# Kernel optimization log

Measured on AMD Instinct MI355X. Metric: run time of the kernel, lower is better.

## Reference

```python
import jax, jax.numpy as jnp
import numpy as np

B, S, D = 4, 4096, 1024
H, HEAD_DIM = 16, 192  # head_dim split into q/k/v of 64 each


def setup_inputs() -> dict:
    key = jax.random.key(0)
    k1, k2 = jax.random.split(key)
    x = jax.random.normal(k1, (B, S, D), dtype=jnp.float32)
    qkv_kernel = jax.random.normal(k2, (D, H, HEAD_DIM), dtype=jnp.float32) * (1.0 / np.sqrt(D))
    qkv_bias = jnp.zeros((H, HEAD_DIM), dtype=jnp.float32)
    return {"x": x, "qkv_kernel": qkv_kernel, "qkv_bias": qkv_bias}


def reference(x, qkv_kernel, qkv_bias):
    # DenseGeneral: [B,S,D] x [D,H,HEAD_DIM] -> [B,S,H,HEAD_DIM]
    qkv = jnp.einsum('bsd,dhf->bshf', x, qkv_kernel) + qkv_bias
    q, k, v = jnp.split(qkv, 3, axis=-1)  # each [B,S,H,64]
    # Faithful to source layout: einsum '...hqd,...hkd' batches over (B,S) and
    # attends across the HEAD axis. With H <= block_size the blockwise loop in
    # the source collapses to this single full softmax over heads.
    scale = 1.0 / jnp.sqrt(jnp.asarray(HEAD_DIM, dtype=q.dtype))  # sqrt(self.head_dim)
    scores = jnp.einsum('bshd,bsgd->bshg', q, k) * scale  # [B,S,H,H]
    weights = jax.nn.softmax(scores, axis=-1)
    out = jnp.einsum('bshg,bsgd->bshd', weights, v)  # [B,S,H,64]
    return out
```

## Files before the change

kernel.cpp:

```cpp
#include <hip/hip_runtime.h>
#include <cstdint>
#include <cstddef>

typedef unsigned short u16;
typedef __attribute__((ext_vector_type(8))) short bf16x8;
typedef __attribute__((ext_vector_type(4))) float f32x4;

__device__ inline float bl(uint32_t u){ union{float f;uint32_t i;}c; c.i = u<<16; return c.f; }
__device__ inline float bh(uint32_t u){ union{float f;uint32_t i;}c; c.i = u & 0xFFFF0000u; return c.f; }
__device__ inline u16 f2bu(float f){
  union{float f;uint32_t u;} c; c.f=f;
  uint32_t u=c.u;
  return (u16)((u + 0x7FFFu + ((u>>16)&1u))>>16);
}

#define GLOAD_LDS16(g, l) __builtin_amdgcn_global_load_lds( \
    (__attribute__((address_space(1))) void*)(g), \
    (__attribute__((address_space(3))) void*)(l), 16, 0, 0)
#define BAR() do{ asm volatile("" ::: "memory"); __builtin_amdgcn_s_barrier(); asm volatile("" ::: "memory"); }while(0)
#define WAIT_LGKM0() do{ asm volatile("s_waitcnt lgkmcnt(0)" ::: "memory"); __builtin_amdgcn_sched_barrier(0); }while(0)

__global__ __launch_bounds__(256) void k_conv_x(const float* __restrict__ X,
                                                u16* __restrict__ Xb, int n4){
  int i = blockIdx.x*256 + threadIdx.x;
  int stride = gridDim.x*256;
  for (; i < n4; i += stride){
    float4 v = ((const float4*)X)[i];
    ushort4 o;
    o.x=f2bu(v.x); o.y=f2bu(v.y); o.z=f2bu(v.z); o.w=f2bu(v.w);
    ((ushort4*)Xb)[i] = o;
  }
}

__global__ __launch_bounds__(256) void k_conv_wt(const float* __restrict__ W,
                                                 u16* __restrict__ Wt){
  __shared__ float t[32][33];
  int n0 = blockIdx.x*32, k0 = blockIdx.y*32;
  int tx = threadIdx.x & 31, ty = threadIdx.x >> 5;
  #pragma unroll
  for (int i=0;i<32;i+=8)
    t[ty+i][tx] = W[(size_t)(k0+ty+i)*3072 + n0+tx];
  __syncthreads();
  #pragma unroll
  for (int i=0;i<32;i+=8)
    Wt[(size_t)(n0+ty+i)*1024 + k0+tx] = f2bu(t[tx][ty+i]);
}

__global__ __launch_bounds__(512, 2) void k_gemm2(const u16* __restrict__ Xb,
                                                  const u16* __restrict__ Wt,
                                                  const float* __restrict__ bias,
                                                  u16* __restrict__ Q){
  __shared__ __align__(16) u16 L[65536];
  const int K = 1024, N = 3072, NT = 32;
  int b = blockIdx.x;
  int swz = (b & 7)*96 + (b >> 3);
  int bm = swz / 12, bn = swz % 12;
  int m0 = bm*256, n0 = bn*256;
  int tid = threadIdx.x, w = tid>>6, lane = tid&63, lr = lane&15, lk = lane>>4;
  int wm = w>>2, wn = w&3;

  f32x4 acc[8][4];
  #pragma unroll
  for (int i=0;i<8;i++)
    #pragma unroll
    for (int j=0;j<4;j++)
      acc[i][j] = (f32x4){0.f,0.f,0.f,0.f};

  int grow = tid>>2;
  int gcol = ((((tid&3)*16) ^ (((tid>>3)&1)<<4) ^ (((tid>>4)&1)<<5)) >> 1);
  const u16* gA0 = Xb + (size_t)(m0 + grow)*K + gcol;
  const u16* gA1 = Xb + (size_t)(m0 + 128 + grow)*K + gcol;
  const u16* gB0 = Wt + (size_t)(n0 + grow)*K + gcol;
  const u16* gB1 = Wt + (size_t)(n0 + 128 + grow)*K + gcol;

#define STG_A(j) do{ int bf=(j)&3, kof=(j)*32; \
    GLOAD_LDS16(gA0+kof, &L[((bf*4+0)<<12) + tid*8]); \
    GLOAD_LDS16(gA1+kof, &L[((bf*4+1)<<12) + tid*8]); }while(0)
#define STG_B(j) do{ int bf=(j)&3, kof=(j)*32; \
    GLOAD_LDS16(gB0+kof, &L[((bf*4+2)<<12) + tid*8]); \
    GLOAD_LDS16(gB1+kof, &L[((bf*4+3)<<12) + tid*8]); }while(0)

  const char* Lb = (const char*)L;
  int colx = (lk*16) ^ (((lr>>1)&3)*16);
  int arow = lr*64 + colx;
  int brow = ((wn&1)*64 + lr)*64 + colx;

  STG_A(0); STG_B(0);
  STG_A(1); STG_B(1);
  STG_A(2); STG_B(2);
  asm volatile("s_waitcnt vmcnt(8)" ::: "memory");
  __builtin_amdgcn_sched_barrier(0);
  BAR();

  for (int t = 0; t < NT; ++t){
    int buf = t & 3;
    int Abase = (buf*4 + wm) << 13;
    int Bbase = (buf*4 + 2 + (wn>>1)) << 13;
    bool st = (t <= NT-4);

    bf16x8 af0, af1, af2, af3, bf0, bf1, bf2, bf3;
    af0 = *(const bf16x8*)(Lb + Abase + 0*1024 + arow);
    af1 = *(const bf16x8*)(Lb + Abase + 1*1024 + arow);
    af2 = *(const bf16x8*)(Lb + Abase + 2*1024 + arow);
    af3 = *(const bf16x8*)(Lb + Abase + 3*1024 + arow);
    bf0 = *(const bf16x8*)(Lb + Bbase + 0*1024 + brow);
    bf1 = *(const bf16x8*)(Lb + Bbase + 1*1024 + brow);
    bf2 = *(const bf16x8*)(Lb + Bbase + 2*1024 + brow);
    bf3 = *(const bf16x8*)(Lb + Bbase + 3*1024 + brow);
    if (st) STG_A(t+3);
    BAR();
    WAIT_LGKM0();
    __builtin_amdgcn_s_setprio(1);
    acc[0][0] = __builtin_amdgcn_mfma_f32_16x16x32_bf16(af0, bf0, acc[0][0], 0,0,0);
    acc[0][1] = __builtin_amdgcn_mfma_f32_16x16x32_bf16(af0, bf1, acc[0][1], 0,0,0);
    acc[0][2] = __builtin_amdgcn_mfma_f32_16x16x32_bf16(af0, bf2, acc[0][2], 0,0,0);
    acc[0][3] = __builtin_amdgcn_mfma_f32_16x16x32_bf16(af0, bf3, acc[0][3], 0,0,0);
    acc[1][0] = __builtin_amdgcn_mfma_f32_16x16x32_bf16(af1, bf0, acc[1][0], 0,0,0);
    acc[1][1] = __builtin_amdgcn_mfma_f32_16x16x32_bf16(af1, bf1, acc[1][1], 0,0,0);
    acc[1][2] = __builtin_amdgcn_mfma_f32_16x16x32_bf16(af1, bf2, acc[1][2], 0,0,0);
    acc[1][3] = __builtin_amdgcn_mfma_f32_16x16x32_bf16(af1, bf3, acc[1][3], 0,0,0);
    acc[2][0] = __builtin_amdgcn_mfma_f32_16x16x32_bf16(af2, bf0, acc[2][0], 0,0,0);
    acc[2][1] = __builtin_amdgcn_mfma_f32_16x16x32_bf16(af2, bf1, acc[2][1], 0,0,0);
    acc[2][2] = __builtin_amdgcn_mfma_f32_16x16x32_bf16(af2, bf2, acc[2][2], 0,0,0);
    acc[2][3] = __builtin_amdgcn_mfma_f32_16x16x32_bf16(af2, bf3, acc[2][3], 0,0,0);
    acc[3][0] = __builtin_amdgcn_mfma_f32_16x16x32_bf16(af3, bf0, acc[3][0], 0,0,0);
    acc[3][1] = __builtin_amdgcn_mfma_f32_16x16x32_bf16(af3, bf1, acc[3][1], 0,0,0);
    acc[3][2] = __builtin_amdgcn_mfma_f32_16x16x32_bf16(af3, bf2, acc[3][2], 0,0,0);
    acc[3][3] = __builtin_amdgcn_mfma_f32_16x16x32_bf16(af3, bf3, acc[3][3], 0,0,0);
    __builtin_amdgcn_s_setprio(0);
    BAR();

    af0 = *(const bf16x8*)(Lb + Abase + 4*1024 + arow);
    af1 = *(const bf16x8*)(Lb + Abase + 5*1024 + arow);
    af2 = *(const bf16x8*)(Lb + Abase + 6*1024 + arow);
    af3 = *(const bf16x8*)(Lb + Abase + 7*1024 + arow);
    if (st) STG_B(t+3);
    BAR();
    WAIT_LGKM0();
    __builtin_amdgcn_s_setprio(1);
    acc[4][0] = __builtin_amdgcn_mfma_f32_16x16x32_bf16(af0, bf0, acc[4][0], 0,0,0);
    acc[4][1] = __builtin_amdgcn_mfma_f32_16x16x32_bf16(af0, bf1, acc[4][1], 0,0,0);
    acc[4][2] = __builtin_amdgcn_mfma_f32_16x16x32_bf16(af0, bf2, acc[4][2], 0,0,0);
    acc[4][3] = __builtin_amdgcn_mfma_f32_16x16x32_bf16(af0, bf3, acc[4][3], 0,0,0);
    acc[5][0] = __builtin_amdgcn_mfma_f32_16x16x32_bf16(af1, bf0, acc[5][0], 0,0,0);
    acc[5][1] = __builtin_amdgcn_mfma_f32_16x16x32_bf16(af1, bf1, acc[5][1], 0,0,0);
    acc[5][2] = __builtin_amdgcn_mfma_f32_16x16x32_bf16(af1, bf2, acc[5][2], 0,0,0);
    acc[5][3] = __builtin_amdgcn_mfma_f32_16x16x32_bf16(af1, bf3, acc[5][3], 0,0,0);
    acc[6][0] = __builtin_amdgcn_mfma_f32_16x16x32_bf16(af2, bf0, acc[6][0], 0,0,0);
    acc[6][1] = __builtin_amdgcn_mfma_f32_16x16x32_bf16(af2, bf1, acc[6][1], 0,0,0);
    acc[6][2] = __builtin_amdgcn_mfma_f32_16x16x32_bf16(af2, bf2, acc[6][2], 0,0,0);
    acc[6][3] = __builtin_amdgcn_mfma_f32_16x16x32_bf16(af2, bf3, acc[6][3], 0,0,0);
    acc[7][0] = __builtin_amdgcn_mfma_f32_16x16x32_bf16(af3, bf0, acc[7][0], 0,0,0);
    acc[7][1] = __builtin_amdgcn_mfma_f32_16x16x32_bf16(af3, bf1, acc[7][1], 0,0,0);
    acc[7][2] = __builtin_amdgcn_mfma_f32_16x16x32_bf16(af3, bf2, acc[7][2], 0,0,0);
    acc[7][3] = __builtin_amdgcn_mfma_f32_16x16x32_bf16(af3, bf3, acc[7][3], 0,0,0);
    __builtin_amdgcn_s_setprio(0);
    if (t <= NT-4)      { asm volatile("s_waitcnt vmcnt(8)" ::: "memory"); }
    else if (t == NT-3) { asm volatile("s_waitcnt vmcnt(4)" ::: "memory"); }
    else if (t == NT-2) { asm volatile("s_waitcnt vmcnt(0)" ::: "memory"); }
    __builtin_amdgcn_sched_barrier(0);
    BAR();
  }
#undef STG_A
#undef STG_B

  {
    u16* reg = &L[w*8192];
    #pragma unroll
    for (int nf=0; nf<4; ++nf){
      int col = nf*16 + lr;
      float bv = bias[n0 + wn*64 + col];
      #pragma unroll
      for (int mi=0; mi<8; ++mi){
        #pragma unroll
        for (int r=0;r<4;r++){
          int rr = mi*16 + lk*4 + r;
          reg[rr*64 + (col ^ ((rr&7)<<3))] = f2bu(acc[mi][nf][r] + bv);
        }
      }
    }
    BAR();
    int co = (tid&31)*8;
    int rgn_c = co>>6;
    int c6 = co&63;
    #pragma unroll
    for (int p=0; p<16; ++p){
      int rI = p*16 + (tid>>5);
      int wreg = ((rI>>7)<<2) + rgn_c;
      int rr = rI & 127;
      const u16* src = &L[wreg*8192 + rr*64 + (c6 ^ ((rr&7)<<3))];
      uint4 v = *(const uint4*)src;
      *(uint4*)&Q[(size_t)(m0+rI)*N + n0 + co] = v;
    }
  }
}

__device__ inline void load16fb(const u16* p, float* f){
  uint4 a = ((const uint4*)p)[0], b4 = ((const uint4*)p)[1];
  f[0]=bl(a.x);  f[1]=bh(a.x);  f[2]=bl(a.y);  f[3]=bh(a.y);
  f[4]=bl(a.z);  f[5]=bh(a.z);  f[6]=bl(a.w);  f[7]=bh(a.w);
  f[8]=bl(b4.x); f[9]=bh(b4.x); f[10]=bl(b4.y);f[11]=bh(b4.y);
  f[12]=bl(b4.z);f[13]=bh(b4.z);f[14]=bl(b4.w);f[15]=bh(b4.w);
}

__global__ __launch_bounds__(256) void k_attn(const u16* __restrict__ Qkv,
                                              float* __restrict__ out){
  __shared__ __align__(16) u16 sm[4][3072];
  int w = threadIdx.x>>6, lane = threadIdx.x&63;
  int token = blockIdx.x*4 + w;
  const uint4* src = (const uint4*)(Qkv + (size_t)token*3072);
  uint4* dst = (uint4*)&sm[w][0];
  for (int i = lane; i < 384; i += 64) dst[i] = src[i];
  __syncthreads();

  int h = lane>>2, dq = lane&3;
  const u16* base = &sm[w][0];
  float qf[16];
  load16fb(base + h*192 + dq*16, qf);

  const float scale = 0.07216878364870323f;
  float s[16];
  #pragma unroll
  for (int g=0; g<16; ++g){
    float kf[16];
    load16fb(base + g*192 + 64 + dq*16, kf);
    float a = 0.f;
    #pragma unroll
    for (int j=0;j<16;j++) a += qf[j]*kf[j];
    a += __shfl_xor(a, 1);
    a += __shfl_xor(a, 2);
    s[g] = a * scale;
  }
  float mx = s[0];
  #pragma unroll
  for (int g=1; g<16; ++g) mx = fmaxf(mx, s[g]);
  float sum = 0.f;
  #pragma unroll
  for (int g=0; g<16; ++g){ s[g] = __expf(s[g]-mx); sum += s[g]; }
  float inv = 1.f/sum;

  float o[16];
  #pragma unroll
  for (int j=0;j<16;j++) o[j] = 0.f;
  #pragma unroll
  for (int g=0; g<16; ++g){
    float wg = s[g]*inv;
    float vf[16];
    load16fb(base + g*192 + 128 + dq*16, vf);
    #pragma unroll
    for (int j=0;j<16;j++) o[j] += wg*vf[j];
  }
  float* op = out + (size_t)token*1024 + h*64 + dq*16;
  #pragma unroll
  for (int i=0;i<4;i++)
    ((float4*)op)[i] = make_float4(o[i*4], o[i*4+1], o[i*4+2], o[i*4+3]);
}

__global__ __launch_bounds__(256) void k_fallback(const float* __restrict__ X,
                                                  const float* __restrict__ W,
                                                  const float* __restrict__ bias,
                                                  float* __restrict__ out){
  int token = blockIdx.x;
  __shared__ float xs[1024];
  __shared__ float qkvs[3072];
  __shared__ float ss[16][16];
  __shared__ float ww[16][16];
  for (int i=threadIdx.x; i<1024; i+=256) xs[i] = X[(size_t)token*1024 + i];
  __syncthreads();
  for (int n=threadIdx.x; n<3072; n+=256){
    float acc = bias[n];
    for (int k=0;k<1024;k++) acc += xs[k]*W[(size_t)k*3072 + n];
    qkvs[n] = acc;
  }
  __syncthreads();
  {
    int t = threadIdx.x, h = t>>4, g = t&15;
    float a = 0.f;
    for (int d=0; d<64; d++) a += qkvs[h*192 + d]*qkvs[g*192 + 64 + d];
    ss[h][g] = a * 0.07216878364870323f;
  }
  __syncthreads();
  if (threadIdx.x < 16){
    int hh = threadIdx.x;
    float m = -1e30f;
    for (int g=0;g<16;g++) m = fmaxf(m, ss[hh][g]);
    float sum = 0.f;
    for (int g=0;g<16;g++){ float e = __expf(ss[hh][g]-m); ww[hh][g]=e; sum+=e; }
    float inv = 1.f/sum;
    for (int g=0;g<16;g++) ww[hh][g] *= inv;
  }
  __syncthreads();
  for (int i=threadIdx.x; i<1024; i+=256){
    int h = i>>6, d = i&63;
    float a = 0.f;
    for (int g=0;g<16;g++) a += ww[h][g]*qkvs[g*192 + 128 + d];
    out[(size_t)token*1024 + i] = a;
  }
}

extern "C" void kernel_launch(void* const* d_in, const int* in_sizes, int n_in,
                              void* d_out, int out_size, void* d_ws, size_t ws_size,
                              hipStream_t stream){
  const float* x    = (const float*)d_in[0];
  const float* wk   = (const float*)d_in[1];
  const float* bias = (const float*)d_in[2];
  float* out = (float*)d_out;

  const size_t offW = 33554432;
  const size_t offQ = offW + 6291456;
  const size_t need = offQ + (size_t)16384*3072*2;

  if (ws_size >= need){
    u16* Xb = (u16*)d_ws;
    u16* Wt = (u16*)((char*)d_ws + offW);
    u16* Q  = (u16*)((char*)d_ws + offQ);
    k_conv_x <<<2048, 256, 0, stream>>>(x, Xb, 16777216/4);
    k_conv_wt<<<dim3(96,32), 256, 0, stream>>>(wk, Wt);
    k_gemm2  <<<768, 512, 0, stream>>>(Xb, Wt, bias, Q);
    k_attn   <<<4096, 256, 0, stream>>>(Q, out);
  } else {
    k_fallback<<<16384, 256, 0, stream>>>(x, wk, bias, out);
  }
}
```

Before: 198.1 us.

## Merge conversion kernels and simplify GEMM main loop to one barrier per k-step

The two fp32-to-bf16 conversion kernels, for X and for the transposed weights, are merged into a single launch that picks its role from the block index, removing one kernel launch and the gap between them. The GEMM inner loop now issues both A and B global-to-LDS prefetches up front, loads all eight A fragments and four B fragments at once, and runs all 32 MFMAs without the two intermediate barriers. This cuts barrier and wait overhead per k-step but holds more fragment registers live and relies on the 4-buffer ring to keep the early stores from clobbering data still being read. An explicit lgkmcnt wait is also added before the epilogue barrier.

```diff
diff --git a/kernel.cpp b/kernel.cpp
--- a/kernel.cpp
+++ b/kernel.cpp
@@ -18,32 +18,33 @@
     (__attribute__((address_space(1))) void*)(g), \
     (__attribute__((address_space(3))) void*)(l), 16, 0, 0)
 #define BAR() do{ asm volatile("" ::: "memory"); __builtin_amdgcn_s_barrier(); asm volatile("" ::: "memory"); }while(0)
-#define WAIT_LGKM0() do{ asm volatile("s_waitcnt lgkmcnt(0)" ::: "memory"); __builtin_amdgcn_sched_barrier(0); }while(0)
-
-__global__ __launch_bounds__(256) void k_conv_x(const float* __restrict__ X,
-                                                u16* __restrict__ Xb, int n4){
-  int i = blockIdx.x*256 + threadIdx.x;
-  int stride = gridDim.x*256;
-  for (; i < n4; i += stride){
-    float4 v = ((const float4*)X)[i];
-    ushort4 o;
-    o.x=f2bu(v.x); o.y=f2bu(v.y); o.z=f2bu(v.z); o.w=f2bu(v.w);
-    ((ushort4*)Xb)[i] = o;
-  }
-}
-
-__global__ __launch_bounds__(256) void k_conv_wt(const float* __restrict__ W,
-                                                 u16* __restrict__ Wt){
+
+__global__ __launch_bounds__(256) void k_conv(const float* __restrict__ X,
+                                              u16* __restrict__ Xb,
+                                              const float* __restrict__ W,
+                                              u16* __restrict__ Wt){
   __shared__ float t[32][33];
-  int n0 = blockIdx.x*32, k0 = blockIdx.y*32;
-  int tx = threadIdx.x & 31, ty = threadIdx.x >> 5;
-  #pragma unroll
-  for (int i=0;i<32;i+=8)
-    t[ty+i][tx] = W[(size_t)(k0+ty+i)*3072 + n0+tx];
-  __syncthreads();
-  #pragma unroll
-  for (int i=0;i<32;i+=8)
-    Wt[(size_t)(n0+ty+i)*1024 + k0+tx] = f2bu(t[tx][ty+i]);
+  int b = blockIdx.x;
+  if (b < 2048){
+    int i = b*256 + threadIdx.x;
+    for (; i < 4194304; i += 2048*256){
+      float4 v = ((const float4*)X)[i];
+      ushort4 o;
+      o.x=f2bu(v.x); o.y=f2bu(v.y); o.z=f2bu(v.z); o.w=f2bu(v.w);
+      ((ushort4*)Xb)[i] = o;
+    }
+  } else {
+    int bb = b - 2048;
+    int n0 = (bb % 96)*32, k0 = (bb / 96)*32;
+    int tx = threadIdx.x & 31, ty = threadIdx.x >> 5;
+    #pragma unroll
+    for (int i=0;i<32;i+=8)
+      t[ty+i][tx] = W[(size_t)(k0+ty+i)*3072 + n0+tx];
+    __syncthreads();
+    #pragma unroll
+    for (int i=0;i<32;i+=8)
+      Wt[(size_t)(n0+ty+i)*1024 + k0+tx] = f2bu(t[tx][ty+i]);
+  }
 }
 
 __global__ __launch_bounds__(512, 2) void k_gemm2(const u16* __restrict__ Xb,
@@ -97,64 +98,58 @@
     int Abase = (buf*4 + wm) << 13;
     int Bbase = (buf*4 + 2 + (wn>>1)) << 13;
     bool st = (t <= NT-4);
-
-    bf16x8 af0, af1, af2, af3, bf0, bf1, bf2, bf3;
-    af0 = *(const bf16x8*)(Lb + Abase + 0*1024 + arow);
-    af1 = *(const bf16x8*)(Lb + Abase + 1*1024 + arow);
-    af2 = *(const bf16x8*)(Lb + Abase + 2*1024 + arow);
-    af3 = *(const bf16x8*)(Lb + Abase + 3*1024 + arow);
-    bf0 = *(const bf16x8*)(Lb + Bbase + 0*1024 + brow);
-    bf1 = *(const bf16x8*)(Lb + Bbase + 1*1024 + brow);
-    bf2 = *(const bf16x8*)(Lb + Bbase + 2*1024 + brow);
-    bf3 = *(const bf16x8*)(Lb + Bbase + 3*1024 + brow);
-    if (st) STG_A(t+3);
-    BAR();
-    WAIT_LGKM0();
+    if (st) { STG_A(t+3); STG_B(t+3); }
+
+    bf16x8 a0,a1,a2,a3,a4,a5,a6,a7, b0,b1,b2,b3;
+    a0 = *(const bf16x8*)(Lb + Abase + 0*1024 + arow);
+    a1 = *(const bf16x8*)(Lb + Abase + 1*1024 + arow);
+    a2 = *(const bf16x8*)(Lb + Abase + 2*1024 + arow);
+    a3 = *(const bf16x8*)(Lb + Abase + 3*1024 + arow);
+    a4 = *(const bf16x8*)(Lb + Abase + 4*1024 + arow);
+    a5 = *(const bf16x8*)(Lb + Abase + 5*1024 + arow);
+    a6 = *(const bf16x8*)(Lb + Abase + 6*1024 + arow);
+    a7 = *(const bf16x8*)(Lb + Abase + 7*1024 + arow);
+    b0 = *(const bf16x8*)(Lb + Bbase + 0*1024 + brow);
+    b1 = *(const bf16x8*)(Lb + Bbase + 1*1024 + brow);
+    b2 = *(const bf16x8*)(Lb + Bbase + 2*1024 + brow);
+    b3 = *(const bf16x8*)(Lb + Bbase + 3*1024 + brow);
+
     __builtin_amdgcn_s_setprio(1);
-    acc[0][0] = __builtin_amdgcn_mfma_f32_16x16x32_bf16(af0, bf0, acc[0][0], 0,0,0);
-    acc[0][1] = __builtin_amdgcn_mfma_f32_16x16x32_bf16(af0, bf1, acc[0][1], 0,0,0);
-    acc[0][2] = __builtin_amdgcn_mfma_f32_16x16x32_bf16(af0, bf2, acc[0][2], 0,0,0);
-    acc[0][3] = __builtin_amdgcn_mfma_f32_16x16x32_bf16(af0, bf3, acc[0][3], 0,0,0);
-    acc[1][0] = __builtin_amdgcn_mfma_f32_16x16x32_bf16(af1, bf0, acc[1][0], 0,0,0);
-    acc[1][1] = __builtin_amdgcn_mfma_f32_16x16x32_bf16(af1, bf1, acc[1][1], 0,0,0);
-    acc[1][2] = __builtin_amdgcn_mfma_f32_16x16x32_bf16(af1, bf2, acc[1][2], 0,0,0);
-    acc[1][3] = __builtin_amdgcn_mfma_f32_16x16x32_bf16(af1, bf3, acc[1][3], 0,0,0);
-    acc[2][0] = __builtin_amdgcn_mfma_f32_16x16x32_bf16(af2, bf0, acc[2][0], 0,0,0);
-    acc[2][1] = __builtin_amdgcn_mfma_f32_16x16x32_bf16(af2, bf1, acc[2][1], 0,0,0);
-    acc[2][2] = __builtin_amdgcn_mfma_f32_16x16x32_bf16(af2, bf2, acc[2][2], 0,0,0);
-    acc[2][3] = __builtin_amdgcn_mfma_f32_16x16x32_bf16(af2, bf3, acc[2][3], 0,0,0);
-    acc[3][0] = __builtin_amdgcn_mfma_f32_16x16x32_bf16(af3, bf0, acc[3][0], 0,0,0);
-    acc[3][1] = __builtin_amdgcn_mfma_f32_16x16x32_bf16(af3, bf1, acc[3][1], 0,0,0);
-    acc[3][2] = __builtin_amdgcn_mfma_f32_16x16x32_bf16(af3, bf2, acc[3][2], 0,0,0);
-    acc[3][3] = __builtin_amdgcn_mfma_f32_16x16x32_bf16(af3, bf3, acc[3][3], 0,0,0);
+    acc[0][0] = __builtin_amdgcn_mfma_f32_16x16x32_bf16(a0, b0, acc[0][0], 0,0,0);
+    acc[0][1] = __builtin_amdgcn_mfma_f32_16x16x32_bf16(a0, b1, acc[0][1], 0,0,0);
+    acc[0][2] = __builtin_amdgcn_mfma_f32_16x16x32_bf16(a0, b2, acc[0][2], 0,0,0);
+    acc[0][3] = __builtin_amdgcn_mfma_f32_16x16x32_bf16(a0, b3, acc[0][3], 0,0,0);
+    acc[1][0] = __builtin_amdgcn_mfma_f32_16x16x32_bf16(a1, b0, acc[1][0], 0,0,0);
+    acc[1][1] = __builtin_amdgcn_mfma_f32_16x16x32_bf16(a1, b1, acc[1][1], 0,0,0);
+    acc[1][2] = __builtin_amdgcn_mfma_f32_16x16x32_bf16(a1, b2, acc[1][2], 0,0,0);
+    acc[1][3] = __builtin_amdgcn_mfma_f32_16x16x32_bf16(a1, b3, acc[1][3], 0,0,0);
+    acc[2][0] = __builtin_amdgcn_mfma_f32_16x16x32_bf16(a2, b0, acc[2][0], 0,0,0);
+    acc[2][1] = __builtin_amdgcn_mfma_f32_16x16x32_bf16(a2, b1, acc[2][1], 0,0,0);
+    acc[2][2] = __builtin_amdgcn_mfma_f32_16x16x32_bf16(a2, b2, acc[2][2], 0,0,0);
+    acc[2][3] = __builtin_amdgcn_mfma_f32_16x16x32_bf16(a2, b3, acc[2][3], 0,0,0);
+    acc[3][0] = __builtin_amdgcn_mfma_f32_16x16x32_bf16(a3, b0, acc[3][0], 0,0,0);
+    acc[3][1] = __builtin_amdgcn_mfma_f32_16x16x32_bf16(a3, b1, acc[3][1], 0,0,0);
+    acc[3][2] = __builtin_amdgcn_mfma_f32_16x16x32_bf16(a3, b2, acc[3][2], 0,0,0);
+    acc[3][3] = __builtin_amdgcn_mfma_f32_16x16x32_bf16(a3, b3, acc[3][3], 0,0,0);
+    acc[4][0] = __builtin_amdgcn_mfma_f32_16x16x32_bf16(a4, b0, acc[4][0], 0,0,0);
+    acc[4][1] = __builtin_amdgcn_mfma_f32_16x16x32_bf16(a4, b1, acc[4][1], 0,0,0);
+    acc[4][2] = __builtin_amdgcn_mfma_f32_16x16x32_bf16(a4, b2, acc[4][2], 0,0,0);
+    acc[4][3] = __builtin_amdgcn_mfma_f32_16x16x32_bf16(a4, b3, acc[4][3], 0,0,0);
+    acc[5][0] = __builtin_amdgcn_mfma_f32_16x16x32_bf16(a5, b0, acc[5][0], 0,0,0);
+    acc[5][1] = __builtin_amdgcn_mfma_f32_16x16x32_bf16(a5, b1, acc[5][1], 0,0,0);
+    acc[5][2] = __builtin_amdgcn_mfma_f32_16x16x32_bf16(a5, b2, acc[5][2], 0,0,0);
+    acc[5][3] = __builtin_amdgcn_mfma_f32_16x16x32_bf16(a5, b3, acc[5][3], 0,0,0);
+    acc[6][0] = __builtin_amdgcn_mfma_f32_16x16x32_bf16(a6, b0, acc[6][0], 0,0,0);
+    acc[6][1] = __builtin_amdgcn_mfma_f32_16x16x32_bf16(a6, b1, acc[6][1], 0,0,0);
+    acc[6][2] = __builtin_amdgcn_mfma_f32_16x16x32_bf16(a6, b2, acc[6][2], 0,0,0);
+    acc[6][3] = __builtin_amdgcn_mfma_f32_16x16x32_bf16(a6, b3, acc[6][3], 0,0,0);
+    acc[7][0] = __builtin_amdgcn_mfma_f32_16x16x32_bf16(a7, b0, acc[7][0], 0,0,0);
+    acc[7][1] = __builtin_amdgcn_mfma_f32_16x16x32_bf16(a7, b1, acc[7][1], 0,0,0);
+    acc[7][2] = __builtin_amdgcn_mfma_f32_16x16x32_bf16(a7, b2, acc[7][2], 0,0,0);
+    acc[7][3] = __builtin_amdgcn_mfma_f32_16x16x32_bf16(a7, b3, acc[7][3], 0,0,0);
     __builtin_amdgcn_s_setprio(0);
-    BAR();
-
-    af0 = *(const bf16x8*)(Lb + Abase + 4*1024 + arow);
-    af1 = *(const bf16x8*)(Lb + Abase + 5*1024 + arow);
-    af2 = *(const bf16x8*)(Lb + Abase + 6*1024 + arow);
-    af3 = *(const bf16x8*)(Lb + Abase + 7*1024 + arow);
-    if (st) STG_B(t+3);
-    BAR();
-    WAIT_LGKM0();
-    __builtin_amdgcn_s_setprio(1);
-    acc[4][0] = __builtin_amdgcn_mfma_f32_16x16x32_bf16(af0, bf0, acc[4][0], 0,0,0);
-    acc[4][1] = __builtin_amdgcn_mfma_f32_16x16x32_bf16(af0, bf1, acc[4][1], 0,0,0);
-    acc[4][2] = __builtin_amdgcn_mfma_f32_16x16x32_bf16(af0, bf2, acc[4][2], 0,0,0);
-    acc[4][3] = __builtin_amdgcn_mfma_f32_16x16x32_bf16(af0, bf3, acc[4][3], 0,0,0);
-    acc[5][0] = __builtin_amdgcn_mfma_f32_16x16x32_bf16(af1, bf0, acc[5][0], 0,0,0);
-    acc[5][1] = __builtin_amdgcn_mfma_f32_16x16x32_bf16(af1, bf1, acc[5][1], 0,0,0);
-    acc[5][2] = __builtin_amdgcn_mfma_f32_16x16x32_bf16(af1, bf2, acc[5][2], 0,0,0);
-    acc[5][3] = __builtin_amdgcn_mfma_f32_16x16x32_bf16(af1, bf3, acc[5][3], 0,0,0);
-    acc[6][0] = __builtin_amdgcn_mfma_f32_16x16x32_bf16(af2, bf0, acc[6][0], 0,0,0);
-    acc[6][1] = __builtin_amdgcn_mfma_f32_16x16x32_bf16(af2, bf1, acc[6][1], 0,0,0);
-    acc[6][2] = __builtin_amdgcn_mfma_f32_16x16x32_bf16(af2, bf2, acc[6][2], 0,0,0);
-    acc[6][3] = __builtin_amdgcn_mfma_f32_16x16x32_bf16(af2, bf3, acc[6][3], 0,0,0);
-    acc[7][0] = __builtin_amdgcn_mfma_f32_16x16x32_bf16(af3, bf0, acc[7][0], 0,0,0);
-    acc[7][1] = __builtin_amdgcn_mfma_f32_16x16x32_bf16(af3, bf1, acc[7][1], 0,0,0);
-    acc[7][2] = __builtin_amdgcn_mfma_f32_16x16x32_bf16(af3, bf2, acc[7][2], 0,0,0);
-    acc[7][3] = __builtin_amdgcn_mfma_f32_16x16x32_bf16(af3, bf3, acc[7][3], 0,0,0);
-    __builtin_amdgcn_s_setprio(0);
+
+    asm volatile("s_waitcnt lgkmcnt(0)" ::: "memory");
     if (t <= NT-4)      { asm volatile("s_waitcnt vmcnt(8)" ::: "memory"); }
     else if (t == NT-3) { asm volatile("s_waitcnt vmcnt(4)" ::: "memory"); }
     else if (t == NT-2) { asm volatile("s_waitcnt vmcnt(0)" ::: "memory"); }
@@ -179,6 +174,7 @@
         }
       }
     }
+    asm volatile("s_waitcnt lgkmcnt(0)" ::: "memory");
     BAR();
     int co = (tid&31)*8;
     int rgn_c = co>>6;
@@ -314,10 +310,9 @@
     u16* Xb = (u16*)d_ws;
     u16* Wt = (u16*)((char*)d_ws + offW);
     u16* Q  = (u16*)((char*)d_ws + offQ);
-    k_conv_x <<<2048, 256, 0, stream>>>(x, Xb, 16777216/4);
-    k_conv_wt<<<dim3(96,32), 256, 0, stream>>>(wk, Wt);
-    k_gemm2  <<<768, 512, 0, stream>>>(Xb, Wt, bias, Q);
-    k_attn   <<<4096, 256, 0, stream>>>(Q, out);
+    k_conv  <<<5120, 256, 0, stream>>>(x, Xb, wk, Wt);
+    k_gemm2 <<<768, 512, 0, stream>>>(Xb, Wt, bias, Q);
+    k_attn  <<<4096, 256, 0, stream>>>(Q, out);
   } else {
     k_fallback<<<16384, 256, 0, stream>>>(x, wk, bias, out);
   }
```

Result: faster. 191.9 us (-3.1%).
